# Performance work log

Hardware: AMD Instinct MI355X
Metric: run time of the kernel (lower is better)

Reference implementation:

```python
import jax, jax.numpy as jnp
import numpy as np

N, T, H, E = 16384, 4, 64, 262144
NEG_SLOPE = 0.2  # LeakyReLU slope for GAT-style attention
LN_EPS = 1e-5


def setup_inputs() -> dict:
    key = jax.random.key(0)
    ks = jax.random.split(key, 24)
    p = {}
    p["pred"] = jax.random.normal(ks[0], (N, T, H), jnp.float32)
    p["ei_structural"] = jax.random.randint(ks[1], (2, E), 0, N, jnp.int32)
    p["ei_functional"] = jax.random.randint(ks[2], (2, E), 0, N, jnp.int32)
    scale = 1.0 / np.sqrt(H)
    i = 3
    for l in range(2):
        for et in ("s", "f"):
            p[f"W{l}{et}"] = (jax.random.normal(ks[i], (H, H), jnp.float32) * scale); i += 1
            p[f"a{l}{et}"] = (jax.random.normal(ks[i], (H,), jnp.float32) * scale); i += 1
        p[f"g{l}"] = jnp.ones((H,), jnp.float32)
        p[f"b{l}"] = jnp.zeros((H,), jnp.float32)
    return p


def _conv(x, ei, W, a, n_dst):
    """Attention-based ST graph conv, temporal_kernel_size=1 (per-step)."""
    h = jnp.einsum('nth,hd->ntd', x, W)          # [N,T,H] linear transform
    src, dst = ei[0], ei[1]
    he = h[src]                                   # [E,T,H] gather per edge
    logits = jax.nn.leaky_relu(jnp.einsum('eth,h->et', he, a), NEG_SLOPE)
    m = jax.ops.segment_max(logits, dst, num_segments=n_dst)     # [N,T]
    ex = jnp.exp(logits - m[dst])                 # stable softmax over incoming edges
    den = jax.ops.segment_sum(ex, dst, num_segments=n_dst)
    alpha = ex / den[dst]                         # [E,T]
    return jax.ops.segment_sum(alpha[..., None] * he, dst, num_segments=n_dst)


def _ln(x, g, b):
    mu = x.mean(-1, keepdims=True)
    v = x.var(-1, keepdims=True)
    return (x - mu) * jax.lax.rsqrt(v + LN_EPS) * g + b


def reference(pred, ei_structural, ei_functional,
              W0s, a0s, W0f, a0f, g0, b0,
              W1s, a1s, W1f, a1f, g1, b1):
    x = pred
    layers = ((W0s, a0s, W0f, a0f, g0, b0), (W1s, a1s, W1f, a1f, g1, b1))
    for (Ws, av, Wf, af, g, b) in layers:
        ms = _conv(x, ei_structural, Ws, av, N)
        mf = _conv(x, ei_functional, Wf, af, N)
        # sum(messages)/len(messages), residual, LayerNorm over H (dropout=identity in eval)
        x = _ln(x + 0.5 * (ms + mf), g, b)
    return x
```

## Files before the change

kernel.cpp:

```cpp
#include <hip/hip_runtime.h>
#include <hip/hip_bf16.h>

#define NN 16384
#define TT 4
#define HH 64
#define NT (NN * TT)
#define CAP 128
#define NEG_SLOPE 0.2f
#define LN_EPS 1e-5f

typedef __attribute__((ext_vector_type(8))) short short8;
typedef __attribute__((ext_vector_type(4))) float f32x4;

__device__ __forceinline__ float bf2f(unsigned short u) {
    return __uint_as_float((unsigned)u << 16);
}
__device__ __forceinline__ unsigned short f2bf(float f) {
    unsigned u = __float_as_uint(f);
    return (unsigned short)((u + 0x7FFF + ((u >> 16) & 1)) >> 16);
}


__global__ __launch_bounds__(256) void prep_kernel(
    const float* __restrict__ W0s_, const float* __restrict__ W0f_,
    const float* __restrict__ W1s_, const float* __restrict__ W1f_,
    short8* __restrict__ wpack, int* __restrict__ cnt2) {
    const int b = blockIdx.x;
    if (b < 128) {
        cnt2[b * 256 + threadIdx.x] = 0;
        return;
    }
    int id = (b - 128) * 256 + threadIdx.x;
    int mat = id >> 9;
    int slot = id & 511;
    int lane = slot & 63;
    int cks = slot >> 6;
    int c = cks >> 1, ks = cks & 1;
    int m = lane & 15, quad = lane >> 4;
    const float* W = (mat == 0) ? W0s_ : (mat == 1) ? W0f_ : (mat == 2) ? W1s_ : W1f_;
    short8 v;
#pragma unroll
    for (int j = 0; j < 8; j++) {
        int k = ks * 32 + quad * 8 + j;
        int n = c * 16 + m;
        v[j] = (short)f2bf(W[k * 64 + n]);
    }
    wpack[id] = v;
}


__device__ __forceinline__ void transform_body(
    int bid, const float4* __restrict__ x4,
    const short8* __restrict__ wp_s, const float* __restrict__ as_,
    const short8* __restrict__ wp_f, const float* __restrict__ af,
    unsigned short* __restrict__ h_s, float* __restrict__ esc_s,
    unsigned short* __restrict__ h_f, float* __restrict__ esc_f) {
    const int lane = threadIdx.x & 63;
    const int wv = threadIdx.x >> 6;
    const int m = lane & 15;
    const int quad = lane >> 4;

    short8 Bs[4][2], Bf[4][2];
#pragma unroll
    for (int c = 0; c < 4; c++) {
#pragma unroll
        for (int ks = 0; ks < 2; ks++) {
            Bs[c][ks] = wp_s[(c * 2 + ks) * 64 + lane];
            Bf[c][ks] = wp_f[(c * 2 + ks) * 64 + lane];
        }
    }
    float a_s[4], a_f[4];
#pragma unroll
    for (int c = 0; c < 4; c++) { a_s[c] = as_[c * 16 + m]; a_f[c] = af[c * 16 + m]; }

    const int rowbase = bid * 128 + wv * 32;
#pragma unroll
    for (int rt = 0; rt < 2; rt++) {
        const int row0 = rowbase + rt * 16;
        const long xbase = (long)(row0 + m) * 16 + quad * 2;
        float4 xa = x4[xbase];
        float4 xb = x4[xbase + 1];
        float4 xc = x4[xbase + 8];
        float4 xd = x4[xbase + 9];
        short8 A0, A1;
        A0[0] = (short)f2bf(xa.x); A0[1] = (short)f2bf(xa.y);
        A0[2] = (short)f2bf(xa.z); A0[3] = (short)f2bf(xa.w);
        A0[4] = (short)f2bf(xb.x); A0[5] = (short)f2bf(xb.y);
        A0[6] = (short)f2bf(xb.z); A0[7] = (short)f2bf(xb.w);
        A1[0] = (short)f2bf(xc.x); A1[1] = (short)f2bf(xc.y);
        A1[2] = (short)f2bf(xc.z); A1[3] = (short)f2bf(xc.w);
        A1[4] = (short)f2bf(xd.x); A1[5] = (short)f2bf(xd.y);
        A1[6] = (short)f2bf(xd.z); A1[7] = (short)f2bf(xd.w);

        f32x4 accs[4], accf[4];
#pragma unroll
        for (int c = 0; c < 4; c++) {
            accs[c] = (f32x4){0.f, 0.f, 0.f, 0.f};
            accf[c] = (f32x4){0.f, 0.f, 0.f, 0.f};
        }
#pragma unroll
        for (int c = 0; c < 4; c++) {
            accs[c] = __builtin_amdgcn_mfma_f32_16x16x32_bf16(A0, Bs[c][0], accs[c], 0, 0, 0);
            accs[c] = __builtin_amdgcn_mfma_f32_16x16x32_bf16(A1, Bs[c][1], accs[c], 0, 0, 0);
            accf[c] = __builtin_amdgcn_mfma_f32_16x16x32_bf16(A0, Bf[c][0], accf[c], 0, 0, 0);
            accf[c] = __builtin_amdgcn_mfma_f32_16x16x32_bf16(A1, Bf[c][1], accf[c], 0, 0, 0);
        }
#pragma unroll
        for (int reg = 0; reg < 4; reg++) {
            const int row = row0 + quad * 4 + reg;
            float ps = 0.f, pf = 0.f;
#pragma unroll
            for (int c = 0; c < 4; c++) {
                h_s[(long)row * 64 + c * 16 + m] = f2bf(accs[c][reg]);
                h_f[(long)row * 64 + c * 16 + m] = f2bf(accf[c][reg]);
                ps = fmaf(accs[c][reg], a_s[c], ps);
                pf = fmaf(accf[c][reg], a_f[c], pf);
            }
#pragma unroll
            for (int off = 1; off < 16; off <<= 1) {
                ps += __shfl_xor(ps, off, 64);
                pf += __shfl_xor(pf, off, 64);
            }
            if (m == 0) {
                float ls = (ps > 0.f) ? ps : NEG_SLOPE * ps;
                float lf = (pf > 0.f) ? pf : NEG_SLOPE * pf;
                esc_s[row] = __expf(ls);
                esc_f[row] = __expf(lf);
            }
        }
    }
}


__global__ __launch_bounds__(256) void st0_kernel(
    const int* __restrict__ ei_s, const int* __restrict__ ei_f, int E,
    int* __restrict__ cnt2, int* __restrict__ col2,
    const float4* __restrict__ pred, const short8* __restrict__ wpack,
    const float* __restrict__ a0s, const float* __restrict__ a0f,
    unsigned short* __restrict__ h_s, float* __restrict__ esc_s,
    unsigned short* __restrict__ h_f, float* __restrict__ esc_f) {
    if (blockIdx.x < 512) {
        transform_body(blockIdx.x, pred, wpack, a0s, wpack + 512, a0f,
                       h_s, esc_s, h_f, esc_f);
        return;
    }
    int e = (blockIdx.x - 512) * 256 + threadIdx.x;
    if (e >= 2 * E) return;
    if (e < E) {
        int d = ei_s[E + e];
        int pos = atomicAdd(&cnt2[d], 1);
        if (pos < CAP) col2[d * CAP + pos] = ei_s[e];
    } else {
        e -= E;
        int d = ei_f[E + e];
        int pos = atomicAdd(&cnt2[NN + d], 1);
        if (pos < CAP) col2[(long)NN * CAP + d * CAP + pos] = ei_f[e];
    }
}


__device__ __forceinline__ float4 aggregate_node(
    int n, int lane, int t,
    const float4* __restrict__ x4,
    const ushort4* __restrict__ hs4, const float* __restrict__ escs,
    const int* __restrict__ cnts, const int* __restrict__ cols,
    const ushort4* __restrict__ hf4, const float* __restrict__ escf,
    const int* __restrict__ cntf, const int* __restrict__ colf,
    float4 gv, float4 bv) {
    int cS = cnts[n]; if (cS > CAP) cS = CAP;
    int cF = cntf[n]; if (cF > CAP) cF = CAP;
    cS = __builtin_amdgcn_readfirstlane(cS);
    cF = __builtin_amdgcn_readfirstlane(cF);
    const int* colS = cols + (long)n * CAP;
    const int* colF = colf + (long)n * CAP;

    int idxS = colS[lane];
    int idxF = colF[lane];
    if (lane >= cS) idxS = 0;
    if (lane >= cF) idxF = 0;

    const int cS64 = cS < 64 ? cS : 64;
    const int cF64 = cF < 64 ? cF : 64;

    float dS = 0.f, sx = 0.f, sy = 0.f, sz = 0.f, sw = 0.f;
    float dF = 0.f, fx = 0.f, fy = 0.f, fz = 0.f, fw = 0.f;

    const int nbS = (cS64 + 7) >> 3;
    const int nbF = (cF64 + 7) >> 3;
    const int nb = nbS > nbF ? nbS : nbF;

    for (int it = 0; it < nb; ++it) {
        const int j = it << 3;
        const bool doS = it < nbS;
        const bool doF = it < nbF;
        int sS[8], sF[8];
        float eS[8], eF[8];
        ushort4 hS[8], hF[8];

        if (doS) {
#pragma unroll
            for (int u = 0; u < 8; u++) sS[u] = __builtin_amdgcn_readlane(idxS, j + u);
#pragma unroll
            for (int u = 0; u < 8; u++) hS[u] = hs4[sS[u] * 64 + lane];
#pragma unroll
            for (int u = 0; u < 8; u++) eS[u] = escs[sS[u] * 4 + t];
        }
        if (doF) {
#pragma unroll
            for (int u = 0; u < 8; u++) sF[u] = __builtin_amdgcn_readlane(idxF, j + u);
#pragma unroll
            for (int u = 0; u < 8; u++) hF[u] = hf4[sF[u] * 64 + lane];
#pragma unroll
            for (int u = 0; u < 8; u++) eF[u] = escf[sF[u] * 4 + t];
        }
        if (doS) {
#pragma unroll
            for (int u = 0; u < 8; u++) {
                float e = (j + u < cS64) ? eS[u] : 0.f;
                dS += e;
                sx = fmaf(e, bf2f(hS[u].x), sx);
                sy = fmaf(e, bf2f(hS[u].y), sy);
                sz = fmaf(e, bf2f(hS[u].z), sz);
                sw = fmaf(e, bf2f(hS[u].w), sw);
            }
        }
        if (doF) {
#pragma unroll
            for (int u = 0; u < 8; u++) {
                float e = (j + u < cF64) ? eF[u] : 0.f;
                dF += e;
                fx = fmaf(e, bf2f(hF[u].x), fx);
                fy = fmaf(e, bf2f(hF[u].y), fy);
                fz = fmaf(e, bf2f(hF[u].z), fz);
                fw = fmaf(e, bf2f(hF[u].w), fw);
            }
        }
    }

    for (int j2 = 64; j2 < cS; ++j2) {
        int s0 = colS[j2];
        float e0 = escs[s0 * 4 + t];
        ushort4 h0 = hs4[(long)s0 * 64 + lane];
        dS += e0;
        sx = fmaf(e0, bf2f(h0.x), sx);
        sy = fmaf(e0, bf2f(h0.y), sy);
        sz = fmaf(e0, bf2f(h0.z), sz);
        sw = fmaf(e0, bf2f(h0.w), sw);
    }
    for (int j2 = 64; j2 < cF; ++j2) {
        int s0 = colF[j2];
        float e0 = escf[s0 * 4 + t];
        ushort4 h0 = hf4[(long)s0 * 64 + lane];
        dF += e0;
        fx = fmaf(e0, bf2f(h0.x), fx);
        fy = fmaf(e0, bf2f(h0.y), fy);
        fz = fmaf(e0, bf2f(h0.z), fz);
        fw = fmaf(e0, bf2f(h0.w), fw);
    }

    float msx = 0.f, msy = 0.f, msz = 0.f, msw = 0.f;
    if (dS > 0.f) {
        float r = 1.f / dS;
        msx = sx * r; msy = sy * r; msz = sz * r; msw = sw * r;
    }
    float mfx = 0.f, mfy = 0.f, mfz = 0.f, mfw = 0.f;
    if (dF > 0.f) {
        float r = 1.f / dF;
        mfx = fx * r; mfy = fy * r; mfz = fz * r; mfw = fw * r;
    }

    float4 xv = x4[(long)n * 64 + lane];
    float v0 = xv.x + 0.5f * (msx + mfx);
    float v1 = xv.y + 0.5f * (msy + mfy);
    float v2 = xv.z + 0.5f * (msz + mfz);
    float v3 = xv.w + 0.5f * (msw + mfw);

    float sum = (v0 + v1) + (v2 + v3);
#pragma unroll
    for (int off = 1; off < 16; off <<= 1) sum += __shfl_xor(sum, off, 64);
    float mu = sum * (1.f / 64.f);
    float d0 = v0 - mu, d1 = v1 - mu, d2 = v2 - mu, d3 = v3 - mu;
    float var = (d0 * d0 + d1 * d1) + (d2 * d2 + d3 * d3);
#pragma unroll
    for (int off = 1; off < 16; off <<= 1) var += __shfl_xor(var, off, 64);
    var *= (1.f / 64.f);
    float inv = rsqrtf(var + LN_EPS);
    float4 o;
    o.x = d0 * inv * gv.x + bv.x;
    o.y = d1 * inv * gv.y + bv.y;
    o.z = d2 * inv * gv.z + bv.z;
    o.w = d3 * inv * gv.w + bv.w;
    return o;
}


__global__ __launch_bounds__(256) void a0t1_kernel(
    const float4* __restrict__ pred,
    const ushort4* __restrict__ hs4, const float* __restrict__ escs,
    const int* __restrict__ cnts, const int* __restrict__ cols,
    const ushort4* __restrict__ hf4, const float* __restrict__ escf,
    const int* __restrict__ cntf, const int* __restrict__ colf,
    const float4* __restrict__ g4, const float4* __restrict__ b4,
    float4* __restrict__ xmid4,
    const short8* __restrict__ wp1s, const short8* __restrict__ wp1f,
    const float* __restrict__ a1s, const float* __restrict__ a1f,
    unsigned short* __restrict__ h1_s, float* __restrict__ esc1_s,
    unsigned short* __restrict__ h1_f, float* __restrict__ esc1_f) {
    __shared__ __align__(16) ushort4 xb4[16][16];
    __shared__ float psumS[4][16];
    __shared__ float psumF[4][16];
    const int wv = threadIdx.x >> 6;
    const int lane = threadIdx.x & 63;
    const int t = lane >> 4;
    const int ci = lane & 15;
    const int n0 = blockIdx.x * 4;
    const int n = n0 + wv;

    float4 o = aggregate_node(n, lane, t, pred, hs4, escs, cnts, cols,
                              hf4, escf, cntf, colf, g4[ci], b4[ci]);
    xmid4[(long)n * 64 + lane] = o;
    ushort4 xu;
    xu.x = f2bf(o.x); xu.y = f2bf(o.y); xu.z = f2bf(o.z); xu.w = f2bf(o.w);
    xb4[wv * 4 + t][ci] = xu;
    __syncthreads();

    const int m = lane & 15;
    const int quad = lane >> 4;
    const short8* xbs8 = (const short8*)xb4;
    short8 A0 = xbs8[m * 8 + quad];
    short8 A1 = xbs8[m * 8 + 4 + quad];
    short8 Bs0 = wp1s[(wv * 2 + 0) * 64 + lane];
    short8 Bs1 = wp1s[(wv * 2 + 1) * 64 + lane];
    short8 Bf0 = wp1f[(wv * 2 + 0) * 64 + lane];
    short8 Bf1 = wp1f[(wv * 2 + 1) * 64 + lane];
    f32x4 accs = (f32x4){0.f, 0.f, 0.f, 0.f};
    f32x4 accf = (f32x4){0.f, 0.f, 0.f, 0.f};
    accs = __builtin_amdgcn_mfma_f32_16x16x32_bf16(A0, Bs0, accs, 0, 0, 0);
    accs = __builtin_amdgcn_mfma_f32_16x16x32_bf16(A1, Bs1, accs, 0, 0, 0);
    accf = __builtin_amdgcn_mfma_f32_16x16x32_bf16(A0, Bf0, accf, 0, 0, 0);
    accf = __builtin_amdgcn_mfma_f32_16x16x32_bf16(A1, Bf1, accf, 0, 0, 0);

    const float av_s = a1s[wv * 16 + m];
    const float av_f = a1f[wv * 16 + m];
#pragma unroll
    for (int reg = 0; reg < 4; reg++) {
        const int row = n0 * 4 + quad * 4 + reg;
        h1_s[(long)row * 64 + wv * 16 + m] = f2bf(accs[reg]);
        h1_f[(long)row * 64 + wv * 16 + m] = f2bf(accf[reg]);
        float pS = accs[reg] * av_s;
        float pF = accf[reg] * av_f;
#pragma unroll
        for (int off = 1; off < 16; off <<= 1) {
            pS += __shfl_xor(pS, off, 64);
            pF += __shfl_xor(pF, off, 64);
        }
        if (m == 0) {
            psumS[wv][quad * 4 + reg] = pS;
            psumF[wv][quad * 4 + reg] = pF;
        }
    }
    __syncthreads();
    if (threadIdx.x < 16) {
        const int r = threadIdx.x;
        float sS = (psumS[0][r] + psumS[1][r]) + (psumS[2][r] + psumS[3][r]);
        float sF = (psumF[0][r] + psumF[1][r]) + (psumF[2][r] + psumF[3][r]);
        float ls = (sS > 0.f) ? sS : NEG_SLOPE * sS;
        float lf = (sF > 0.f) ? sF : NEG_SLOPE * sF;
        esc1_s[n0 * 4 + r] = __expf(ls);
        esc1_f[n0 * 4 + r] = __expf(lf);
    }
}


__global__ __launch_bounds__(256) void a1_kernel(
    const float4* __restrict__ x4,
    const ushort4* __restrict__ hs4, const float* __restrict__ escs,
    const int* __restrict__ cnts, const int* __restrict__ cols,
    const ushort4* __restrict__ hf4, const float* __restrict__ escf,
    const int* __restrict__ cntf, const int* __restrict__ colf,
    const float4* __restrict__ g4, const float4* __restrict__ b4,
    float4* __restrict__ out4) {
    const int wv = threadIdx.x >> 6;
    const int lane = threadIdx.x & 63;
    const int t = lane >> 4;
    const int ci = lane & 15;
    const int n = blockIdx.x * 4 + wv;
    float4 o = aggregate_node(n, lane, t, x4, hs4, escs, cnts, cols,
                              hf4, escf, cntf, colf, g4[ci], b4[ci]);
    out4[(long)n * 64 + lane] = o;
}


extern "C" void kernel_launch(void* const* d_in, const int* in_sizes, int n_in,
                              void* d_out, int out_size, void* d_ws, size_t ws_size,
                              hipStream_t stream) {
    const float* pred = (const float*)d_in[0];
    const int* ei_s = (const int*)d_in[1];
    const int* ei_f = (const int*)d_in[2];
    const float* W0s = (const float*)d_in[3];
    const float* a0s = (const float*)d_in[4];
    const float* W0f = (const float*)d_in[5];
    const float* a0f = (const float*)d_in[6];
    const float* g0  = (const float*)d_in[7];
    const float* b0  = (const float*)d_in[8];
    const float* W1s = (const float*)d_in[9];
    const float* a1s = (const float*)d_in[10];
    const float* W1f = (const float*)d_in[11];
    const float* a1f = (const float*)d_in[12];
    const float* g1  = (const float*)d_in[13];
    const float* b1  = (const float*)d_in[14];
    const int E = in_sizes[1] / 2;

    char* ws = (char*)d_ws;
    auto alloc = [&](size_t bytes) {
        char* p = ws;
        ws += (bytes + 255) & ~(size_t)255;
        return p;
    };
    int* cnt2 = (int*)alloc((size_t)2 * NN * sizeof(int));
    int* col2 = (int*)alloc((size_t)2 * NN * CAP * sizeof(int));
    short8* wpack = (short8*)alloc((size_t)4 * 512 * sizeof(short8));
    unsigned short* h0_s = (unsigned short*)alloc((size_t)NT * HH * sizeof(unsigned short));
    unsigned short* h0_f = (unsigned short*)alloc((size_t)NT * HH * sizeof(unsigned short));
    unsigned short* h1_s = (unsigned short*)alloc((size_t)NT * HH * sizeof(unsigned short));
    unsigned short* h1_f = (unsigned short*)alloc((size_t)NT * HH * sizeof(unsigned short));
    float* esc0_s = (float*)alloc((size_t)NT * sizeof(float));
    float* esc0_f = (float*)alloc((size_t)NT * sizeof(float));
    float* esc1_s = (float*)alloc((size_t)NT * sizeof(float));
    float* esc1_f = (float*)alloc((size_t)NT * sizeof(float));
    float* x_mid = (float*)alloc((size_t)NT * HH * sizeof(float));

    const int* cnt_s = cnt2;
    const int* cnt_f = cnt2 + NN;
    const int* col_s = col2;
    const int* col_f = col2 + (size_t)NN * CAP;

    const int SB = (2 * E + 255) / 256;

    prep_kernel<<<136, 256, 0, stream>>>(W0s, W0f, W1s, W1f, wpack, cnt2);

    st0_kernel<<<512 + SB, 256, 0, stream>>>(
        ei_s, ei_f, E, cnt2, col2,
        (const float4*)pred, wpack, a0s, a0f,
        h0_s, esc0_s, h0_f, esc0_f);

    a0t1_kernel<<<NN / 4, 256, 0, stream>>>(
        (const float4*)pred,
        (const ushort4*)h0_s, esc0_s, cnt_s, col_s,
        (const ushort4*)h0_f, esc0_f, cnt_f, col_f,
        (const float4*)g0, (const float4*)b0,
        (float4*)x_mid,
        wpack + 1024, wpack + 1536, a1s, a1f,
        h1_s, esc1_s, h1_f, esc1_f);

    a1_kernel<<<NN / 4, 256, 0, stream>>>(
        (const float4*)x_mid,
        (const ushort4*)h1_s, esc1_s, cnt_s, col_s,
        (const ushort4*)h1_f, esc1_f, cnt_f, col_f,
        (const float4*)g1, (const float4*)b1, (float4*)d_out);
}
```

Before: 216.1 us.

## Process two destination nodes per wavefront in aggregation kernels

Each wavefront now aggregates two destination nodes, interleaving four gather streams with a 4-wide unroll instead of two streams with an 8-wide unroll. The a0t1 kernel runs its bf16 MFMA projection over two 16-row tiles per block, reusing the loaded weight fragments, and pads the shared staging buffer. Grids are halved. This is meant to amortise per-wave setup and raise memory-level parallelism on irregular gathers. The cost is more register pressure and load imbalance when the two nodes have different degrees.

```diff
diff --git a/kernel.cpp b/kernel.cpp
--- a/kernel.cpp
+++ b/kernel.cpp
@@ -159,138 +159,213 @@
 }
 
 
-__device__ __forceinline__ float4 aggregate_node(
-    int n, int lane, int t,
+__device__ __forceinline__ void aggregate_pair(
+    int nA, int nB, int lane, int t,
     const float4* __restrict__ x4,
     const ushort4* __restrict__ hs4, const float* __restrict__ escs,
     const int* __restrict__ cnts, const int* __restrict__ cols,
     const ushort4* __restrict__ hf4, const float* __restrict__ escf,
     const int* __restrict__ cntf, const int* __restrict__ colf,
-    float4 gv, float4 bv) {
-    int cS = cnts[n]; if (cS > CAP) cS = CAP;
-    int cF = cntf[n]; if (cF > CAP) cF = CAP;
-    cS = __builtin_amdgcn_readfirstlane(cS);
-    cF = __builtin_amdgcn_readfirstlane(cF);
-    const int* colS = cols + (long)n * CAP;
-    const int* colF = colf + (long)n * CAP;
-
-    int idxS = colS[lane];
-    int idxF = colF[lane];
-    if (lane >= cS) idxS = 0;
-    if (lane >= cF) idxF = 0;
-
-    const int cS64 = cS < 64 ? cS : 64;
-    const int cF64 = cF < 64 ? cF : 64;
-
-    float dS = 0.f, sx = 0.f, sy = 0.f, sz = 0.f, sw = 0.f;
-    float dF = 0.f, fx = 0.f, fy = 0.f, fz = 0.f, fw = 0.f;
-
-    const int nbS = (cS64 + 7) >> 3;
-    const int nbF = (cF64 + 7) >> 3;
-    const int nb = nbS > nbF ? nbS : nbF;
+    float4 gv, float4 bv, float4& oA, float4& oB) {
+    int cSA = cnts[nA]; if (cSA > CAP) cSA = CAP;
+    int cFA = cntf[nA]; if (cFA > CAP) cFA = CAP;
+    int cSB = cnts[nB]; if (cSB > CAP) cSB = CAP;
+    int cFB = cntf[nB]; if (cFB > CAP) cFB = CAP;
+    cSA = __builtin_amdgcn_readfirstlane(cSA);
+    cFA = __builtin_amdgcn_readfirstlane(cFA);
+    cSB = __builtin_amdgcn_readfirstlane(cSB);
+    cFB = __builtin_amdgcn_readfirstlane(cFB);
+    const int* colSA = cols + (long)nA * CAP;
+    const int* colFA = colf + (long)nA * CAP;
+    const int* colSB = cols + (long)nB * CAP;
+    const int* colFB = colf + (long)nB * CAP;
+
+    int idxSA = colSA[lane]; if (lane >= cSA) idxSA = 0;
+    int idxFA = colFA[lane]; if (lane >= cFA) idxFA = 0;
+    int idxSB = colSB[lane]; if (lane >= cSB) idxSB = 0;
+    int idxFB = colFB[lane]; if (lane >= cFB) idxFB = 0;
+
+    const int cSA64 = cSA < 64 ? cSA : 64;
+    const int cFA64 = cFA < 64 ? cFA : 64;
+    const int cSB64 = cSB < 64 ? cSB : 64;
+    const int cFB64 = cFB < 64 ? cFB : 64;
+
+    float dSA = 0.f, sxA = 0.f, syA = 0.f, szA = 0.f, swA = 0.f;
+    float dFA = 0.f, fxA = 0.f, fyA = 0.f, fzA = 0.f, fwA = 0.f;
+    float dSB = 0.f, sxB = 0.f, syB = 0.f, szB = 0.f, swB = 0.f;
+    float dFB = 0.f, fxB = 0.f, fyB = 0.f, fzB = 0.f, fwB = 0.f;
+
+    const int nbSA = (cSA64 + 3) >> 2;
+    const int nbFA = (cFA64 + 3) >> 2;
+    const int nbSB = (cSB64 + 3) >> 2;
+    const int nbFB = (cFB64 + 3) >> 2;
+    int nb = nbSA;
+    if (nbFA > nb) nb = nbFA;
+    if (nbSB > nb) nb = nbSB;
+    if (nbFB > nb) nb = nbFB;
 
     for (int it = 0; it < nb; ++it) {
-        const int j = it << 3;
-        const bool doS = it < nbS;
-        const bool doF = it < nbF;
-        int sS[8], sF[8];
-        float eS[8], eF[8];
-        ushort4 hS[8], hF[8];
-
-        if (doS) {
-#pragma unroll
-            for (int u = 0; u < 8; u++) sS[u] = __builtin_amdgcn_readlane(idxS, j + u);
-#pragma unroll
-            for (int u = 0; u < 8; u++) hS[u] = hs4[sS[u] * 64 + lane];
-#pragma unroll
-            for (int u = 0; u < 8; u++) eS[u] = escs[sS[u] * 4 + t];
-        }
-        if (doF) {
-#pragma unroll
-            for (int u = 0; u < 8; u++) sF[u] = __builtin_amdgcn_readlane(idxF, j + u);
-#pragma unroll
-            for (int u = 0; u < 8; u++) hF[u] = hf4[sF[u] * 64 + lane];
-#pragma unroll
-            for (int u = 0; u < 8; u++) eF[u] = escf[sF[u] * 4 + t];
-        }
-        if (doS) {
-#pragma unroll
-            for (int u = 0; u < 8; u++) {
-                float e = (j + u < cS64) ? eS[u] : 0.f;
-                dS += e;
-                sx = fmaf(e, bf2f(hS[u].x), sx);
-                sy = fmaf(e, bf2f(hS[u].y), sy);
-                sz = fmaf(e, bf2f(hS[u].z), sz);
-                sw = fmaf(e, bf2f(hS[u].w), sw);
-            }
-        }
-        if (doF) {
-#pragma unroll
-            for (int u = 0; u < 8; u++) {
-                float e = (j + u < cF64) ? eF[u] : 0.f;
-                dF += e;
-                fx = fmaf(e, bf2f(hF[u].x), fx);
-                fy = fmaf(e, bf2f(hF[u].y), fy);
-                fz = fmaf(e, bf2f(hF[u].z), fz);
-                fw = fmaf(e, bf2f(hF[u].w), fw);
-            }
-        }
-    }
-
-    for (int j2 = 64; j2 < cS; ++j2) {
-        int s0 = colS[j2];
+        const int j = it << 2;
+        const bool doSA = it < nbSA, doFA = it < nbFA;
+        const bool doSB = it < nbSB, doFB = it < nbFB;
+        int sSA[4], sFA[4], sSB[4], sFB[4];
+        float eSA[4], eFA[4], eSB[4], eFB[4];
+        ushort4 hSA[4], hFA[4], hSB[4], hFB[4];
+
+        if (doSA) {
+#pragma unroll
+            for (int u = 0; u < 4; u++) sSA[u] = __builtin_amdgcn_readlane(idxSA, j + u);
+#pragma unroll
+            for (int u = 0; u < 4; u++) hSA[u] = hs4[sSA[u] * 64 + lane];
+#pragma unroll
+            for (int u = 0; u < 4; u++) eSA[u] = escs[sSA[u] * 4 + t];
+        }
+        if (doFA) {
+#pragma unroll
+            for (int u = 0; u < 4; u++) sFA[u] = __builtin_amdgcn_readlane(idxFA, j + u);
+#pragma unroll
+            for (int u = 0; u < 4; u++) hFA[u] = hf4[sFA[u] * 64 + lane];
+#pragma unroll
+            for (int u = 0; u < 4; u++) eFA[u] = escf[sFA[u] * 4 + t];
+        }
+        if (doSB) {
+#pragma unroll
+            for (int u = 0; u < 4; u++) sSB[u] = __builtin_amdgcn_readlane(idxSB, j + u);
+#pragma unroll
+            for (int u = 0; u < 4; u++) hSB[u] = hs4[sSB[u] * 64 + lane];
+#pragma unroll
+            for (int u = 0; u < 4; u++) eSB[u] = escs[sSB[u] * 4 + t];
+        }
+        if (doFB) {
+#pragma unroll
+            for (int u = 0; u < 4; u++) sFB[u] = __builtin_amdgcn_readlane(idxFB, j + u);
+#pragma unroll
+            for (int u = 0; u < 4; u++) hFB[u] = hf4[sFB[u] * 64 + lane];
+#pragma unroll
+            for (int u = 0; u < 4; u++) eFB[u] = escf[sFB[u] * 4 + t];
+        }
+        if (doSA) {
+#pragma unroll
+            for (int u = 0; u < 4; u++) {
+                float e = (j + u < cSA64) ? eSA[u] : 0.f;
+                dSA += e;
+                sxA = fmaf(e, bf2f(hSA[u].x), sxA);
+                syA = fmaf(e, bf2f(hSA[u].y), syA);
+                szA = fmaf(e, bf2f(hSA[u].z), szA);
+                swA = fmaf(e, bf2f(hSA[u].w), swA);
+            }
+        }
+        if (doFA) {
+#pragma unroll
+            for (int u = 0; u < 4; u++) {
+                float e = (j + u < cFA64) ? eFA[u] : 0.f;
+                dFA += e;
+                fxA = fmaf(e, bf2f(hFA[u].x), fxA);
+                fyA = fmaf(e, bf2f(hFA[u].y), fyA);
+                fzA = fmaf(e, bf2f(hFA[u].z), fzA);
+                fwA = fmaf(e, bf2f(hFA[u].w), fwA);
+            }
+        }
+        if (doSB) {
+#pragma unroll
+            for (int u = 0; u < 4; u++) {
+                float e = (j + u < cSB64) ? eSB[u] : 0.f;
+                dSB += e;
+                sxB = fmaf(e, bf2f(hSB[u].x), sxB);
+                syB = fmaf(e, bf2f(hSB[u].y), syB);
+                szB = fmaf(e, bf2f(hSB[u].z), szB);
+                swB = fmaf(e, bf2f(hSB[u].w), swB);
+            }
+        }
+        if (doFB) {
+#pragma unroll
+            for (int u = 0; u < 4; u++) {
+                float e = (j + u < cFB64) ? eFB[u] : 0.f;
+                dFB += e;
+                fxB = fmaf(e, bf2f(hFB[u].x), fxB);
+                fyB = fmaf(e, bf2f(hFB[u].y), fyB);
+                fzB = fmaf(e, bf2f(hFB[u].z), fzB);
+                fwB = fmaf(e, bf2f(hFB[u].w), fwB);
+            }
+        }
+    }
+
+    for (int j2 = 64; j2 < cSA; ++j2) {
+        int s0 = colSA[j2];
         float e0 = escs[s0 * 4 + t];
         ushort4 h0 = hs4[(long)s0 * 64 + lane];
-        dS += e0;
-        sx = fmaf(e0, bf2f(h0.x), sx);
-        sy = fmaf(e0, bf2f(h0.y), sy);
-        sz = fmaf(e0, bf2f(h0.z), sz);
-        sw = fmaf(e0, bf2f(h0.w), sw);
-    }
-    for (int j2 = 64; j2 < cF; ++j2) {
-        int s0 = colF[j2];
+        dSA += e0;
+        sxA = fmaf(e0, bf2f(h0.x), sxA); syA = fmaf(e0, bf2f(h0.y), syA);
+        szA = fmaf(e0, bf2f(h0.z), szA); swA = fmaf(e0, bf2f(h0.w), swA);
+    }
+    for (int j2 = 64; j2 < cFA; ++j2) {
+        int s0 = colFA[j2];
         float e0 = escf[s0 * 4 + t];
         ushort4 h0 = hf4[(long)s0 * 64 + lane];
-        dF += e0;
-        fx = fmaf(e0, bf2f(h0.x), fx);
-        fy = fmaf(e0, bf2f(h0.y), fy);
-        fz = fmaf(e0, bf2f(h0.z), fz);
-        fw = fmaf(e0, bf2f(h0.w), fw);
-    }
-
-    float msx = 0.f, msy = 0.f, msz = 0.f, msw = 0.f;
-    if (dS > 0.f) {
-        float r = 1.f / dS;
-        msx = sx * r; msy = sy * r; msz = sz * r; msw = sw * r;
-    }
-    float mfx = 0.f, mfy = 0.f, mfz = 0.f, mfw = 0.f;
-    if (dF > 0.f) {
-        float r = 1.f / dF;
-        mfx = fx * r; mfy = fy * r; mfz = fz * r; mfw = fw * r;
-    }
-
-    float4 xv = x4[(long)n * 64 + lane];
-    float v0 = xv.x + 0.5f * (msx + mfx);
-    float v1 = xv.y + 0.5f * (msy + mfy);
-    float v2 = xv.z + 0.5f * (msz + mfz);
-    float v3 = xv.w + 0.5f * (msw + mfw);
-
-    float sum = (v0 + v1) + (v2 + v3);
-#pragma unroll
-    for (int off = 1; off < 16; off <<= 1) sum += __shfl_xor(sum, off, 64);
-    float mu = sum * (1.f / 64.f);
-    float d0 = v0 - mu, d1 = v1 - mu, d2 = v2 - mu, d3 = v3 - mu;
-    float var = (d0 * d0 + d1 * d1) + (d2 * d2 + d3 * d3);
-#pragma unroll
-    for (int off = 1; off < 16; off <<= 1) var += __shfl_xor(var, off, 64);
-    var *= (1.f / 64.f);
-    float inv = rsqrtf(var + LN_EPS);
-    float4 o;
-    o.x = d0 * inv * gv.x + bv.x;
-    o.y = d1 * inv * gv.y + bv.y;
-    o.z = d2 * inv * gv.z + bv.z;
-    o.w = d3 * inv * gv.w + bv.w;
-    return o;
+        dFA += e0;
+        fxA = fmaf(e0, bf2f(h0.x), fxA); fyA = fmaf(e0, bf2f(h0.y), fyA);
+        fzA = fmaf(e0, bf2f(h0.z), fzA); fwA = fmaf(e0, bf2f(h0.w), fwA);
+    }
+    for (int j2 = 64; j2 < cSB; ++j2) {
+        int s0 = colSB[j2];
+        float e0 = escs[s0 * 4 + t];
+        ushort4 h0 = hs4[(long)s0 * 64 + lane];
+        dSB += e0;
+        sxB = fmaf(e0, bf2f(h0.x), sxB); syB = fmaf(e0, bf2f(h0.y), syB);
+        szB = fmaf(e0, bf2f(h0.z), szB); swB = fmaf(e0, bf2f(h0.w), swB);
+    }
+    for (int j2 = 64; j2 < cFB; ++j2) {
+        int s0 = colFB[j2];
+        float e0 = escf[s0 * 4 + t];
+        ushort4 h0 = hf4[(long)s0 * 64 + lane];
+        dFB += e0;
+        fxB = fmaf(e0, bf2f(h0.x), fxB); fyB = fmaf(e0, bf2f(h0.y), fyB);
+        fzB = fmaf(e0, bf2f(h0.z), fzB); fwB = fmaf(e0, bf2f(h0.w), fwB);
+    }
+
+    float msxA = 0.f, msyA = 0.f, mszA = 0.f, mswA = 0.f;
+    if (dSA > 0.f) { float r = 1.f / dSA; msxA = sxA * r; msyA = syA * r; mszA = szA * r; mswA = swA * r; }
+    float mfxA = 0.f, mfyA = 0.f, mfzA = 0.f, mfwA = 0.f;
+    if (dFA > 0.f) { float r = 1.f / dFA; mfxA = fxA * r; mfyA = fyA * r; mfzA = fzA * r; mfwA = fwA * r; }
+    float msxB = 0.f, msyB = 0.f, mszB = 0.f, mswB = 0.f;
+    if (dSB > 0.f) { float r = 1.f / dSB; msxB = sxB * r; msyB = syB * r; mszB = szB * r; mswB = swB * r; }
+    float mfxB = 0.f, mfyB = 0.f, mfzB = 0.f, mfwB = 0.f;
+    if (dFB > 0.f) { float r = 1.f / dFB; mfxB = fxB * r; mfyB = fyB * r; mfzB = fzB * r; mfwB = fwB * r; }
+
+    float4 xvA = x4[(long)nA * 64 + lane];
+    float4 xvB = x4[(long)nB * 64 + lane];
+    float a0 = xvA.x + 0.5f * (msxA + mfxA);
+    float a1 = xvA.y + 0.5f * (msyA + mfyA);
+    float a2 = xvA.z + 0.5f * (mszA + mfzA);
+    float a3 = xvA.w + 0.5f * (mswA + mfwA);
+    float b0 = xvB.x + 0.5f * (msxB + mfxB);
+    float b1 = xvB.y + 0.5f * (msyB + mfyB);
+    float b2 = xvB.z + 0.5f * (mszB + mfzB);
+    float b3 = xvB.w + 0.5f * (mswB + mfwB);
+
+    float sumA = (a0 + a1) + (a2 + a3);
+    float sumB = (b0 + b1) + (b2 + b3);
+#pragma unroll
+    for (int off = 1; off < 16; off <<= 1) {
+        sumA += __shfl_xor(sumA, off, 64);
+        sumB += __shfl_xor(sumB, off, 64);
+    }
+    float muA = sumA * (1.f / 64.f), muB = sumB * (1.f / 64.f);
+    float dA0 = a0 - muA, dA1 = a1 - muA, dA2 = a2 - muA, dA3 = a3 - muA;
+    float dB0 = b0 - muB, dB1 = b1 - muB, dB2 = b2 - muB, dB3 = b3 - muB;
+    float varA = (dA0 * dA0 + dA1 * dA1) + (dA2 * dA2 + dA3 * dA3);
+    float varB = (dB0 * dB0 + dB1 * dB1) + (dB2 * dB2 + dB3 * dB3);
+#pragma unroll
+    for (int off = 1; off < 16; off <<= 1) {
+        varA += __shfl_xor(varA, off, 64);
+        varB += __shfl_xor(varB, off, 64);
+    }
+    float invA = rsqrtf(varA * (1.f / 64.f) + LN_EPS);
+    float invB = rsqrtf(varB * (1.f / 64.f) + LN_EPS);
+    oA.x = dA0 * invA * gv.x + bv.x; oA.y = dA1 * invA * gv.y + bv.y;
+    oA.z = dA2 * invA * gv.z + bv.z; oA.w = dA3 * invA * gv.w + bv.w;
+    oB.x = dB0 * invB * gv.x + bv.x; oB.y = dB1 * invB * gv.y + bv.y;
+    oB.z = dB2 * invB * gv.z + bv.z; oB.w = dB3 * invB * gv.w + bv.w;
 }
 
 
@@ -306,68 +381,74 @@
     const float* __restrict__ a1s, const float* __restrict__ a1f,
     unsigned short* __restrict__ h1_s, float* __restrict__ esc1_s,
     unsigned short* __restrict__ h1_f, float* __restrict__ esc1_f) {
-    __shared__ __align__(16) ushort4 xb4[16][16];
-    __shared__ float psumS[4][16];
-    __shared__ float psumF[4][16];
+    __shared__ __align__(16) ushort4 xb4[32][18];
+    __shared__ float psumS[4][2][16];
+    __shared__ float psumF[4][2][16];
     const int wv = threadIdx.x >> 6;
     const int lane = threadIdx.x & 63;
     const int t = lane >> 4;
     const int ci = lane & 15;
-    const int n0 = blockIdx.x * 4;
-    const int n = n0 + wv;
-
-    float4 o = aggregate_node(n, lane, t, pred, hs4, escs, cnts, cols,
-                              hf4, escf, cntf, colf, g4[ci], b4[ci]);
-    xmid4[(long)n * 64 + lane] = o;
-    ushort4 xu;
-    xu.x = f2bf(o.x); xu.y = f2bf(o.y); xu.z = f2bf(o.z); xu.w = f2bf(o.w);
-    xb4[wv * 4 + t][ci] = xu;
+    const int n0 = blockIdx.x * 8;
+    const int nA = n0 + wv * 2, nB = nA + 1;
+
+    float4 oA, oB;
+    aggregate_pair(nA, nB, lane, t, pred, hs4, escs, cnts, cols,
+                   hf4, escf, cntf, colf, g4[ci], b4[ci], oA, oB);
+    xmid4[(long)nA * 64 + lane] = oA;
+    xmid4[(long)nB * 64 + lane] = oB;
+    ushort4 xuA, xuB;
+    xuA.x = f2bf(oA.x); xuA.y = f2bf(oA.y); xuA.z = f2bf(oA.z); xuA.w = f2bf(oA.w);
+    xuB.x = f2bf(oB.x); xuB.y = f2bf(oB.y); xuB.z = f2bf(oB.z); xuB.w = f2bf(oB.w);
+    xb4[wv * 8 + t][ci] = xuA;
+    xb4[wv * 8 + 4 + t][ci] = xuB;
     __syncthreads();
 
     const int m = lane & 15;
     const int quad = lane >> 4;
     const short8* xbs8 = (const short8*)xb4;
-    short8 A0 = xbs8[m * 8 + quad];
-    short8 A1 = xbs8[m * 8 + 4 + quad];
     short8 Bs0 = wp1s[(wv * 2 + 0) * 64 + lane];
     short8 Bs1 = wp1s[(wv * 2 + 1) * 64 + lane];
     short8 Bf0 = wp1f[(wv * 2 + 0) * 64 + lane];
     short8 Bf1 = wp1f[(wv * 2 + 1) * 64 + lane];
-    f32x4 accs = (f32x4){0.f, 0.f, 0.f, 0.f};
-    f32x4 accf = (f32x4){0.f, 0.f, 0.f, 0.f};
-    accs = __builtin_amdgcn_mfma_f32_16x16x32_bf16(A0, Bs0, accs, 0, 0, 0);
-    accs = __builtin_amdgcn_mfma_f32_16x16x32_bf16(A1, Bs1, accs, 0, 0, 0);
-    accf = __builtin_amdgcn_mfma_f32_16x16x32_bf16(A0, Bf0, accf, 0, 0, 0);
-    accf = __builtin_amdgcn_mfma_f32_16x16x32_bf16(A1, Bf1, accf, 0, 0, 0);
-
     const float av_s = a1s[wv * 16 + m];
     const float av_f = a1f[wv * 16 + m];
 #pragma unroll
-    for (int reg = 0; reg < 4; reg++) {
-        const int row = n0 * 4 + quad * 4 + reg;
-        h1_s[(long)row * 64 + wv * 16 + m] = f2bf(accs[reg]);
-        h1_f[(long)row * 64 + wv * 16 + m] = f2bf(accf[reg]);
-        float pS = accs[reg] * av_s;
-        float pF = accf[reg] * av_f;
-#pragma unroll
-        for (int off = 1; off < 16; off <<= 1) {
-            pS += __shfl_xor(pS, off, 64);
-            pF += __shfl_xor(pF, off, 64);
-        }
-        if (m == 0) {
-            psumS[wv][quad * 4 + reg] = pS;
-            psumF[wv][quad * 4 + reg] = pF;
+    for (int tt = 0; tt < 2; ++tt) {
+        short8 A0 = xbs8[(tt * 16 + m) * 9 + quad];
+        short8 A1 = xbs8[(tt * 16 + m) * 9 + 4 + quad];
+        f32x4 accs = (f32x4){0.f, 0.f, 0.f, 0.f};
+        f32x4 accf = (f32x4){0.f, 0.f, 0.f, 0.f};
+        accs = __builtin_amdgcn_mfma_f32_16x16x32_bf16(A0, Bs0, accs, 0, 0, 0);
+        accs = __builtin_amdgcn_mfma_f32_16x16x32_bf16(A1, Bs1, accs, 0, 0, 0);
+        accf = __builtin_amdgcn_mfma_f32_16x16x32_bf16(A0, Bf0, accf, 0, 0, 0);
+        accf = __builtin_amdgcn_mfma_f32_16x16x32_bf16(A1, Bf1, accf, 0, 0, 0);
+#pragma unroll
+        for (int reg = 0; reg < 4; reg++) {
+            const int row = n0 * 4 + tt * 16 + quad * 4 + reg;
+            h1_s[(long)row * 64 + wv * 16 + m] = f2bf(accs[reg]);
+            h1_f[(long)row * 64 + wv * 16 + m] = f2bf(accf[reg]);
+            float pS = accs[reg] * av_s;
+            float pF = accf[reg] * av_f;
+#pragma unroll
+            for (int off = 1; off < 16; off <<= 1) {
+                pS += __shfl_xor(pS, off, 64);
+                pF += __shfl_xor(pF, off, 64);
+            }
+            if (m == 0) {
+                psumS[wv][tt][quad * 4 + reg] = pS;
+                psumF[wv][tt][quad * 4 + reg] = pF;
+            }
         }
     }
     __syncthreads();
-    if (threadIdx.x < 16) {
-        const int r = threadIdx.x;
-        float sS = (psumS[0][r] + psumS[1][r]) + (psumS[2][r] + psumS[3][r]);
-        float sF = (psumF[0][r] + psumF[1][r]) + (psumF[2][r] + psumF[3][r]);
+    if (threadIdx.x < 32) {
+        const int r = threadIdx.x & 15, tt = threadIdx.x >> 4;
+        float sS = (psumS[0][tt][r] + psumS[1][tt][r]) + (psumS[2][tt][r] + psumS[3][tt][r]);
+        float sF = (psumF[0][tt][r] + psumF[1][tt][r]) + (psumF[2][tt][r] + psumF[3][tt][r]);
         float ls = (sS > 0.f) ? sS : NEG_SLOPE * sS;
         float lf = (sF > 0.f) ? sF : NEG_SLOPE * sF;
-        esc1_s[n0 * 4 + r] = __expf(ls);
-        esc1_f[n0 * 4 + r] = __expf(lf);
+        esc1_s[n0 * 4 + tt * 16 + r] = __expf(ls);
+        esc1_f[n0 * 4 + tt * 16 + r] = __expf(lf);
     }
 }
 
@@ -384,10 +465,12 @@
     const int lane = threadIdx.x & 63;
     const int t = lane >> 4;
     const int ci = lane & 15;
-    const int n = blockIdx.x * 4 + wv;
-    float4 o = aggregate_node(n, lane, t, x4, hs4, escs, cnts, cols,
-                              hf4, escf, cntf, colf, g4[ci], b4[ci]);
-    out4[(long)n * 64 + lane] = o;
+    const int nA = blockIdx.x * 8 + wv * 2, nB = nA + 1;
+    float4 oA, oB;
+    aggregate_pair(nA, nB, lane, t, x4, hs4, escs, cnts, cols,
+                   hf4, escf, cntf, colf, g4[ci], b4[ci], oA, oB);
+    out4[(long)nA * 64 + lane] = oA;
+    out4[(long)nB * 64 + lane] = oB;
 }
 
 
@@ -444,7 +527,7 @@
         (const float4*)pred, wpack, a0s, a0f,
         h0_s, esc0_s, h0_f, esc0_f);
 
-    a0t1_kernel<<<NN / 4, 256, 0, stream>>>(
+    a0t1_kernel<<<NN / 8, 256, 0, stream>>>(
         (const float4*)pred,
         (const ushort4*)h0_s, esc0_s, cnt_s, col_s,
         (const ushort4*)h0_f, esc0_f, cnt_f, col_f,
@@ -453,7 +536,7 @@
         wpack + 1024, wpack + 1536, a1s, a1f,
         h1_s, esc1_s, h1_f, esc1_f);
 
-    a1_kernel<<<NN / 4, 256, 0, stream>>>(
+    a1_kernel<<<NN / 8, 256, 0, stream>>>(
         (const float4*)x_mid,
         (const ushort4*)h1_s, esc1_s, cnt_s, col_s,
         (const ushort4*)h1_f, esc1_f, cnt_f, col_f,
```

Result: no change. 217.9 us (+0.8%).
